# Optimization experiments

Hardware: AMD Instinct MI355X
Metric: run time of the kernel (lower is better)

## Reference

```python
import jax, jax.numpy as jnp
import numpy as np

B, L, D = 4, 4096, 8
K_MAX = 64


def _pack_codes(x):
    # binary_quantize (x > 0) then pack the d sign bits into one int32 code.
    bits = (x > 0).astype(jnp.int32)                       # [B, L, d]
    powers = 2 ** jnp.arange(x.shape[-1], dtype=jnp.int32)  # [d]
    return jnp.einsum('bld,d->bl', bits, powers)           # [B, L]


def setup_inputs() -> dict:
    key = jax.random.key(0)
    kq, kk = jax.random.split(key)
    return {
        'query_up': jax.random.normal(kq, (B, L, D), dtype=jnp.float32),
        'key_up': jax.random.normal(kk, (B, L, D), dtype=jnp.float32),
        'head_idx': 0,
    }


def reference(query_up, key_up, head_idx):
    # Wu-Manber matches the first prefix_len sign bits; the Trie matches the
    # full sign-bit vector, so their set intersection is exactly the set of
    # keys whose full binary signature equals the query's.
    Lq = query_up.shape[1]
    q_codes = _pack_codes(query_up)   # [B, L]
    k_codes = _pack_codes(key_up)     # [B, L]
    match = q_codes[:, :, None] == k_codes[:, None, :]     # [B, L, L] bool
    # score = key index j if it matches, else L (sentinel); smallest K_MAX
    # scores = first K_MAX matching key indices in ascending order.
    idx = jnp.arange(Lq, dtype=jnp.int32)
    score = jnp.where(match, idx[None, None, :], jnp.int32(Lq))  # [B, L, L]
    neg_top, _ = jax.lax.top_k(-score, K_MAX)              # [B, L, K_MAX]
    cand = -neg_top                                        # ascending matches, then L pads
    cand = jnp.where(cand < Lq, cand, -1)                  # pad with -1 like torch.full
    # merge_candidate_indices_groups: cat (single group) -> sort -> take k_max.
    # torch.sort puts the -1 padding first; unique_consecutive over full
    # [B, L] slices is an identity here (no two whole slices coincide).
    return jnp.sort(cand, axis=-1).astype(jnp.int64)       # [B, L, K_MAX]
```

## Files before the change

### kernel.cpp

```cpp
#include <hip/hip_runtime.h>

#define BB      4
#define LL      4096
#define DD      8
#define KMAX    64
#define NCODES  256

__global__ void __launch_bounds__(1024)
build_res(const float* __restrict__ key_up, int* __restrict__ res) {
    __shared__ int scodes[LL];
    __shared__ int sbuf[16][KMAX];

    const int b = blockIdx.x >> 4;
    const int g = blockIdx.x & 15;
    const int t = threadIdx.x;

    const float4* kp = reinterpret_cast<const float4*>(key_up + (size_t)b * LL * DD);
#pragma unroll
    for (int j = 0; j < 4; ++j) {
        int k = t + j * 1024;
        float4 a = kp[k * 2];
        float4 c4 = kp[k * 2 + 1];
        int code = ((int)(a.x > 0.f))
                 | ((int)(a.y > 0.f) << 1)
                 | ((int)(a.z > 0.f) << 2)
                 | ((int)(a.w > 0.f) << 3)
                 | ((int)(c4.x > 0.f) << 4)
                 | ((int)(c4.y > 0.f) << 5)
                 | ((int)(c4.z > 0.f) << 6)
                 | ((int)(c4.w > 0.f) << 7);
        scodes[k] = code;
    }
    __syncthreads();

    const int w    = t >> 6;
    const int lane = t & 63;
    const int c    = g * 16 + w;

    int v[64];
#pragma unroll
    for (int i = 0; i < 64; ++i) v[i] = scodes[i * 64 + lane];

    const unsigned long long prefix = (1ull << lane) - 1ull;
    int found = 0;
#pragma unroll
    for (int i = 0; i < 64; ++i) {
        bool m = (v[i] == c);
        unsigned long long mask = __ballot(m);
        if (m) {
            int rank = found + (int)__popcll(mask & prefix);
            if (rank < KMAX) sbuf[w][rank] = i * 64 + lane;
        }
        found += (int)__popcll(mask);
    }
    int mcount = found < KMAX ? found : KMAX;
    int pad    = KMAX - mcount;
    int val    = (lane < pad) ? -1 : sbuf[w][lane - pad];
    res[((size_t)b * NCODES + c) * KMAX + lane] = val;
}

__global__ void gather_out(const float* __restrict__ query_up,
                           const int* __restrict__ res,
                           int* __restrict__ out) {
    int tid  = blockIdx.x * blockDim.x + threadIdx.x;
    int lane = threadIdx.x & 63;
    int wq   = tid >> 6;
    int myq  = wq * 4 + (lane >> 4);
    int b    = myq >> 12;
    float x  = query_up[(size_t)myq * DD + (lane & 7)];
    unsigned long long mask = __ballot(x > 0.f);
    int code = (int)((mask >> ((lane >> 4) << 4)) & 0xffull);
    const int4* src = reinterpret_cast<const int4*>(res + ((size_t)b * NCODES + code) * KMAX);
    int4 vv = src[lane & 15];
    reinterpret_cast<int4*>(out)[(size_t)myq * 16 + (lane & 15)] = vv;
}

extern "C" void kernel_launch(void* const* d_in, const int* in_sizes, int n_in,
                              void* d_out, int out_size, void* d_ws, size_t ws_size,
                              hipStream_t stream) {
    const float* query_up = (const float*)d_in[0];
    const float* key_up   = (const float*)d_in[1];

    int* out = (int*)d_out;
    int* res = (int*)d_ws;

    build_res<<<BB * 16, 1024, 0, stream>>>(key_up, res);
    gather_out<<<(BB * LL * 16) / 256, 256, 0, stream>>>(query_up, res, out);
}
```

Baseline: 65.51 us.

## Fuse table build and gather into one cooperative kernel with grid sync

Merges the per-code candidate table construction and the query gather into a single cooperative kernel launched with 256 blocks of 1024 threads. The first 64 blocks build the table, then every block does a grid-wide sync before handling its share of queries. This removes one kernel launch and the gap between launches, at the cost of a grid barrier and of needing all 256 large blocks to be co-resident. It also drops the register preload of the 64 shared-memory codes and reads them inside the scan loop instead.

```diff
diff --git a/kernel.cpp b/kernel.cpp
--- a/kernel.cpp
+++ b/kernel.cpp
@@ -1,4 +1,7 @@
 #include <hip/hip_runtime.h>
+#include <hip/hip_cooperative_groups.h>
+
+namespace cg = cooperative_groups;
 
 #define BB      4
 #define LL      4096
@@ -7,70 +10,70 @@
 #define NCODES  256
 
 __global__ void __launch_bounds__(1024)
-build_res(const float* __restrict__ key_up, int* __restrict__ res) {
+fused_candidates(const float* __restrict__ query_up,
+                 const float* __restrict__ key_up,
+                 int* __restrict__ res,
+                 int* __restrict__ out) {
     __shared__ int scodes[LL];
     __shared__ int sbuf[16][KMAX];
 
-    const int b = blockIdx.x >> 4;
-    const int g = blockIdx.x & 15;
-    const int t = threadIdx.x;
+    const int t    = threadIdx.x;
+    const int lane = t & 63;
+    const int w    = t >> 6;
 
-    const float4* kp = reinterpret_cast<const float4*>(key_up + (size_t)b * LL * DD);
+    if (blockIdx.x < BB * 16) {
+        const int b = blockIdx.x >> 4;
+        const int g = blockIdx.x & 15;
+
+        const float4* kp = reinterpret_cast<const float4*>(key_up + (size_t)b * LL * DD);
 #pragma unroll
-    for (int j = 0; j < 4; ++j) {
-        int k = t + j * 1024;
-        float4 a = kp[k * 2];
-        float4 c4 = kp[k * 2 + 1];
-        int code = ((int)(a.x > 0.f))
-                 | ((int)(a.y > 0.f) << 1)
-                 | ((int)(a.z > 0.f) << 2)
-                 | ((int)(a.w > 0.f) << 3)
-                 | ((int)(c4.x > 0.f) << 4)
-                 | ((int)(c4.y > 0.f) << 5)
-                 | ((int)(c4.z > 0.f) << 6)
-                 | ((int)(c4.w > 0.f) << 7);
-        scodes[k] = code;
+        for (int j = 0; j < 4; ++j) {
+            int k = t + j * 1024;
+            float4 a  = kp[k * 2];
+            float4 c4 = kp[k * 2 + 1];
+            int code = ((int)(a.x  > 0.f))
+                     | ((int)(a.y  > 0.f) << 1)
+                     | ((int)(a.z  > 0.f) << 2)
+                     | ((int)(a.w  > 0.f) << 3)
+                     | ((int)(c4.x > 0.f) << 4)
+                     | ((int)(c4.y > 0.f) << 5)
+                     | ((int)(c4.z > 0.f) << 6)
+                     | ((int)(c4.w > 0.f) << 7);
+            scodes[k] = code;
+        }
+        __syncthreads();
+
+        const int c = g * 16 + w;
+        const unsigned long long prefix = (1ull << lane) - 1ull;
+        int found = 0;
+#pragma unroll
+        for (int i = 0; i < 64; ++i) {
+            int  vi = scodes[i * 64 + lane];
+            bool m  = (vi == c);
+            unsigned long long mask = __ballot(m);
+            if (m) {
+                int rank = found + (int)__popcll(mask & prefix);
+                if (rank < KMAX) sbuf[w][rank] = i * 64 + lane;
+            }
+            found += (int)__popcll(mask);
+        }
+        int mcount = found < KMAX ? found : KMAX;
+        int pad    = KMAX - mcount;
+        int val    = (lane < pad) ? -1 : sbuf[w][lane - pad];
+        res[((size_t)b * NCODES + c) * KMAX + lane] = val;
     }
-    __syncthreads();
 
-    const int w    = t >> 6;
-    const int lane = t & 63;
-    const int c    = g * 16 + w;
+    __threadfence();
+    cg::this_grid().sync();
 
-    int v[64];
-#pragma unroll
-    for (int i = 0; i < 64; ++i) v[i] = scodes[i * 64 + lane];
-
-    const unsigned long long prefix = (1ull << lane) - 1ull;
-    int found = 0;
-#pragma unroll
-    for (int i = 0; i < 64; ++i) {
-        bool m = (v[i] == c);
-        unsigned long long mask = __ballot(m);
-        if (m) {
-            int rank = found + (int)__popcll(mask & prefix);
-            if (rank < KMAX) sbuf[w][rank] = i * 64 + lane;
-        }
-        found += (int)__popcll(mask);
-    }
-    int mcount = found < KMAX ? found : KMAX;
-    int pad    = KMAX - mcount;
-    int val    = (lane < pad) ? -1 : sbuf[w][lane - pad];
-    res[((size_t)b * NCODES + c) * KMAX + lane] = val;
-}
-
-__global__ void gather_out(const float* __restrict__ query_up,
-                           const int* __restrict__ res,
-                           int* __restrict__ out) {
-    int tid  = blockIdx.x * blockDim.x + threadIdx.x;
-    int lane = threadIdx.x & 63;
-    int wq   = tid >> 6;
+    int gtid = blockIdx.x * 1024 + t;
+    int wq   = gtid >> 6;
     int myq  = wq * 4 + (lane >> 4);
-    int b    = myq >> 12;
+    int b2   = myq >> 12;
     float x  = query_up[(size_t)myq * DD + (lane & 7)];
     unsigned long long mask = __ballot(x > 0.f);
     int code = (int)((mask >> ((lane >> 4) << 4)) & 0xffull);
-    const int4* src = reinterpret_cast<const int4*>(res + ((size_t)b * NCODES + code) * KMAX);
+    const int4* src = reinterpret_cast<const int4*>(res + ((size_t)b2 * NCODES + code) * KMAX);
     int4 vv = src[lane & 15];
     reinterpret_cast<int4*>(out)[(size_t)myq * 16 + (lane & 15)] = vv;
 }
@@ -84,6 +87,7 @@
     int* out = (int*)d_out;
     int* res = (int*)d_ws;
 
-    build_res<<<BB * 16, 1024, 0, stream>>>(key_up, res);
-    gather_out<<<(BB * LL * 16) / 256, 256, 0, stream>>>(query_up, res, out);
+    void* args[] = { (void*)&query_up, (void*)&key_up, (void*)&res, (void*)&out };
+    hipLaunchCooperativeKernel((const void*)fused_candidates,
+                               dim3(256), dim3(1024), args, 0, stream);
 }
```

New measurement: 183.4 us. 2.8x slower.
